# Performance work log

Measured on AMD Instinct MI355X. Metric: run time of the kernel, lower is better.

The kernel has to match this reference:

```python
import jax, jax.numpy as jnp
import numpy as np

DIM = 512
HEADS = 8
HEAD_DIM = DIM // HEADS
WINDOW = 128
TOKEN_SELF_ATTN_VALUE = -5e4  # lucidrains local-attention constant for shared_qk self mask


def setup_inputs() -> dict:
    key = jax.random.key(0)
    k1, k2, k3, k4 = jax.random.split(key, 4)
    B, N = 4, 8192
    x = jax.random.normal(k1, (B, N, DIM), dtype=jnp.float32)
    w_qkv = jax.random.normal(k2, (3 * DIM, DIM), dtype=jnp.float32) * (DIM ** -0.5)
    w_proj = jax.random.normal(k3, (DIM, DIM), dtype=jnp.float32) * (DIM ** -0.5)
    b_proj = jax.random.normal(k4, (DIM,), dtype=jnp.float32) * 0.01
    return {"x": x, "w_qkv": w_qkv, "w_proj": w_proj, "b_proj": b_proj}


def _look_around(b):
    # b: [B,H,nw,w,D] -> [B,H,nw,2w,D] = concat(prev_window, cur_window); window 0 padded with zeros
    padded = jnp.pad(b, ((0, 0), (0, 0), (1, 0), (0, 0), (0, 0)))
    return jnp.concatenate([padded[:, :, :-1], b], axis=3)


def _local_attn(q, k, v):
    # causal sliding-window attention, window=128, look_backward=1, shared_qk
    B, H, N, D = q.shape
    w = WINDOW
    nw = N // w
    scale = D ** -0.5
    # shared_qk: l2-normalize keys (F.normalize, eps=1e-12)
    k = k / jnp.clip(jnp.linalg.norm(k, axis=-1, keepdims=True), 1e-12, None)

    bq = q.reshape(B, H, nw, w, D)
    bk = _look_around(k.reshape(B, H, nw, w, D))  # [B,H,nw,2w,D]
    bv = _look_around(v.reshape(B, H, nw, w, D))

    t = jnp.arange(N).reshape(nw, w)
    t_pad = jnp.pad(t, ((1, 0), (0, 0)), constant_values=-1)
    bq_t = t                                         # [nw, w]
    bq_k = jnp.concatenate([t_pad[:-1], t], axis=1)  # [nw, 2w]

    sim = jnp.einsum('bhwie,bhwje->bhwij', bq, bk) * scale  # [B,H,nw,w,2w]

    self_mask = bq_t[:, :, None] == bq_k[:, None, :]
    causal_mask = bq_t[:, :, None] < bq_k[:, None, :]
    pad_mask = (bq_k == -1)[:, None, :]
    mask_value = -jnp.finfo(sim.dtype).max
    sim = jnp.where(self_mask, TOKEN_SELF_ATTN_VALUE, sim)
    sim = jnp.where(causal_mask | pad_mask, mask_value, sim)

    attn = jax.nn.softmax(sim, axis=-1)  # dropout is identity in eval mode
    out = jnp.einsum('bhwij,bhwje->bhwie', attn, bv)
    return out.reshape(B, H, N, D)


def reference(x, w_qkv, w_proj, b_proj):
    B, N, C = x.shape
    qkv = x @ w_qkv.T  # [B,N,3C]
    q, k, v = jnp.split(qkv, 3, axis=-1)
    to_heads = lambda t: t.reshape(B, N, HEADS, HEAD_DIM).transpose(0, 2, 1, 3)
    out = _local_attn(to_heads(q), to_heads(k), to_heads(v))  # [B,H,N,D]
    out = out.transpose(0, 2, 1, 3).reshape(B, N, C)
    return out @ w_proj.T + b_proj
```

## Files before the change

### kernel.cpp

```cpp
#include <hip/hip_runtime.h>
#include <stdint.h>

typedef uint16_t u16;
typedef __bf16 bf16x8 __attribute__((ext_vector_type(8)));
typedef float f32x4 __attribute__((ext_vector_type(4)));
typedef uint16_t u16x4 __attribute__((ext_vector_type(4)));
typedef uint16_t u16x8 __attribute__((ext_vector_type(8)));

typedef __attribute__((address_space(1))) void as1_void;
typedef __attribute__((address_space(3))) void as3_void;

__device__ __forceinline__ float bf2f(u16 b) {
    union { uint32_t u; float f; } v; v.u = ((uint32_t)b) << 16; return v.f;
}
__device__ __forceinline__ u16 f2bf(float f) {
    union { float f; uint32_t u; } v; v.f = f;
    uint32_t u = v.u;
    u += 0x7fffu + ((u >> 16) & 1u);
    return (u16)(u >> 16);
}
__device__ __forceinline__ void gload_lds16(const u16* g, u16* l) {
    __builtin_amdgcn_global_load_lds((as1_void*)g, (as3_void*)l, 16, 0, 0);
}

__global__ __launch_bounds__(256) void cvt3(
    const float* __restrict__ x,  u16* __restrict__ xb,
    const float* __restrict__ wq, u16* __restrict__ wqb,
    const float* __restrict__ wp, u16* __restrict__ wpb)
{
    const float* src; u16* dst; int base, nb;
    const int b = blockIdx.x;
    if (b < 1024)      { src = x;  dst = xb;  base = b;        nb = 1024; }
    else if (b < 1072) { src = wq; dst = wqb; base = b - 1024; nb = 48;   }
    else               { src = wp; dst = wpb; base = b - 1072; nb = 16;   }
    size_t i = ((size_t)base * 256 + threadIdx.x) * 8;
    const size_t stride = (size_t)nb * 256 * 8;
    #pragma unroll
    for (int it = 0; it < 8; ++it, i += stride) {
        f32x4 a = *(const f32x4*)(src + i);
        f32x4 c = *(const f32x4*)(src + i + 4);
        u16x8 o;
        o[0] = f2bf(a[0]); o[1] = f2bf(a[1]); o[2] = f2bf(a[2]); o[3] = f2bf(a[3]);
        o[4] = f2bf(c[0]); o[5] = f2bf(c[1]); o[6] = f2bf(c[2]); o[7] = f2bf(c[3]);
        *(u16x8*)(dst + i) = o;
    }
}

template<int NT, bool C_F32, bool NORMK>
__global__ __launch_bounds__(512) void gemm256(
    const u16* __restrict__ A, int lda,
    const u16* __restrict__ B, int ldb,
    const float* __restrict__ bias,
    void* __restrict__ Cv, int ldc)
{
    __shared__ u16 lA[2][256 * 64];
    __shared__ u16 lB[2][256 * 64];

    const int tid  = threadIdx.x;
    const int lane = tid & 63;
    const int wave = tid >> 6;
    const int wm = wave >> 2;
    const int wn = wave & 3;
    const int cl = lane & 15;
    const int gr = lane >> 4;

    int fid = blockIdx.y * gridDim.x + blockIdx.x;
    const int nwg = gridDim.x * gridDim.y;
    fid = (fid & 7) * (nwg >> 3) + (fid >> 3);
    const int row0 = (fid / gridDim.x) * 256;
    const int col0 = (fid % gridDim.x) * 256;

    const int srow   = lane >> 3;
    const int schunk = ((lane & 7) - srow) & 7;

    f32x4 acc[8][4] = {};

    auto STAGE = [&](int t, int d) {
        const int k0 = t * 64;
        #pragma unroll
        for (int i = 0; i < 4; ++i) {
            const int Rg = wave * 32 + i * 8;
            gload_lds16(A + (size_t)(row0 + Rg + srow) * lda + k0 + schunk * 8,
                        &lA[d][Rg * 64]);
            gload_lds16(B + (size_t)(col0 + Rg + srow) * ldb + k0 + schunk * 8,
                        &lB[d][Rg * 64]);
        }
    };

    auto COMPUTE = [&](int d) {
        const u16* la = lA[d];
        const u16* lb = lB[d];
        bf16x8 bfrag[2][4];
        #pragma unroll
        for (int kk = 0; kk < 2; ++kk)
            #pragma unroll
            for (int n = 0; n < 4; ++n) {
                const int rb = wn * 64 + n * 16 + cl;
                bfrag[kk][n] = *(const bf16x8*)(lb + rb * 64 + (((kk * 4 + gr + rb) & 7) * 8));
            }
        __builtin_amdgcn_s_setprio(1);
        #pragma unroll
        for (int m = 0; m < 8; ++m) {
            const int ra = wm * 128 + m * 16 + cl;
            const bf16x8 a0 = *(const bf16x8*)(la + ra * 64 + (((gr + ra) & 7) * 8));
            const bf16x8 a1 = *(const bf16x8*)(la + ra * 64 + (((4 + gr + ra) & 7) * 8));
            #pragma unroll
            for (int n = 0; n < 4; ++n)
                acc[m][n] = __builtin_amdgcn_mfma_f32_16x16x32_bf16(a0, bfrag[0][n], acc[m][n], 0, 0, 0);
            #pragma unroll
            for (int n = 0; n < 4; ++n)
                acc[m][n] = __builtin_amdgcn_mfma_f32_16x16x32_bf16(a1, bfrag[1][n], acc[m][n], 0, 0, 0);
        }
        __builtin_amdgcn_s_setprio(0);
    };

    STAGE(0, 0);
    STAGE(1, 1);
    #pragma unroll
    for (int t = 0; t < NT; ++t) {
        if (t < NT - 1) asm volatile("s_waitcnt vmcnt(8)" ::: "memory");
        else            asm volatile("s_waitcnt vmcnt(0)" ::: "memory");
        __builtin_amdgcn_s_barrier();
        COMPUTE(t & 1);
        __builtin_amdgcn_s_barrier();
        if (t + 2 < NT) STAGE(t + 2, t & 1);
    }

    if constexpr (NORMK) {
        if (col0 >= 512 && col0 < 1024) {
            #pragma unroll
            for (int m = 0; m < 8; ++m)
                #pragma unroll
                for (int j = 0; j < 4; ++j) {
                    float ss = 0.f;
                    #pragma unroll
                    for (int n = 0; n < 4; ++n) ss += acc[m][n][j] * acc[m][n][j];
                    ss += __shfl_xor(ss, 1);
                    ss += __shfl_xor(ss, 2);
                    ss += __shfl_xor(ss, 4);
                    ss += __shfl_xor(ss, 8);
                    const float scl = 1.f / fmaxf(sqrtf(ss), 1e-12f);
                    #pragma unroll
                    for (int n = 0; n < 4; ++n) acc[m][n][j] *= scl;
                }
        }
    }

    #pragma unroll
    for (int m = 0; m < 8; ++m) {
        const int r = row0 + wm * 128 + m * 16 + gr * 4;
        #pragma unroll
        for (int n = 0; n < 4; ++n) {
            const int c = col0 + wn * 64 + n * 16 + cl;
            const float bv = bias ? bias[c] : 0.f;
            #pragma unroll
            for (int j = 0; j < 4; ++j) {
                const float val = acc[m][n][j] + bv;
                if constexpr (C_F32) ((float*)Cv)[(size_t)(r + j) * ldc + c] = val;
                else                 ((u16*)Cv)[(size_t)(r + j) * ldc + c] = f2bf(val);
            }
        }
    }
}

template<bool A_F32, bool C_F32, bool NORMK>
__global__ __launch_bounds__(256) void gemm_bt_f32(
    const void* __restrict__ Av, int lda,
    const float* __restrict__ B, int ldb,
    const float* __restrict__ bias,
    void* __restrict__ Cv, int ldc,
    int K)
{
    __shared__ u16 lA[128 * 32];
    __shared__ u16 lB[128 * 32];

    const int tid  = threadIdx.x;
    const int lane = tid & 63;
    const int wave = tid >> 6;
    const int wr   = (wave >> 1) * 64;
    const int wc   = (wave & 1) * 64;
    const int row0 = blockIdx.y * 128;
    const int col0 = blockIdx.x * 128;

    f32x4 acc[4][4] = {};

    for (int k0 = 0; k0 < K; k0 += 32) {
        #pragma unroll
        for (int i = 0; i < 4; ++i) {
            const int idx = i * 256 + tid;
            const int r = idx >> 3;
            const int p = (idx & 7) * 4;
            u16x4 a4, b4;
            if constexpr (A_F32) {
                const float* Af = (const float*)Av;
                f32x4 va = *(const f32x4*)(Af + (size_t)(row0 + r) * lda + k0 + p);
                a4[0] = f2bf(va[0]); a4[1] = f2bf(va[1]); a4[2] = f2bf(va[2]); a4[3] = f2bf(va[3]);
            } else {
                const u16* Ab = (const u16*)Av;
                a4 = *(const u16x4*)(Ab + (size_t)(row0 + r) * lda + k0 + p);
            }
            {
                f32x4 vb = *(const f32x4*)(B + (size_t)(col0 + r) * ldb + k0 + p);
                b4[0] = f2bf(vb[0]); b4[1] = f2bf(vb[1]); b4[2] = f2bf(vb[2]); b4[3] = f2bf(vb[3]);
            }
            *(u16x4*)&lA[r * 32 + p] = a4;
            *(u16x4*)&lB[r * 32 + p] = b4;
        }
        __syncthreads();

        bf16x8 af[4], bfv[4];
        #pragma unroll
        for (int m = 0; m < 4; ++m)
            af[m] = *(const bf16x8*)(lA + (wr + m * 16 + (lane & 15)) * 32 + (lane >> 4) * 8);
        #pragma unroll
        for (int n = 0; n < 4; ++n)
            bfv[n] = *(const bf16x8*)(lB + (wc + n * 16 + (lane & 15)) * 32 + (lane >> 4) * 8);
        #pragma unroll
        for (int m = 0; m < 4; ++m)
            #pragma unroll
            for (int n = 0; n < 4; ++n)
                acc[m][n] = __builtin_amdgcn_mfma_f32_16x16x32_bf16(af[m], bfv[n], acc[m][n], 0, 0, 0);
        __syncthreads();
    }

    if constexpr (NORMK) {
        if (col0 >= 512 && col0 < 1024) {
            #pragma unroll
            for (int m = 0; m < 4; ++m)
                #pragma unroll
                for (int j = 0; j < 4; ++j) {
                    float ss = 0.f;
                    #pragma unroll
                    for (int n = 0; n < 4; ++n) ss += acc[m][n][j] * acc[m][n][j];
                    ss += __shfl_xor(ss, 1);
                    ss += __shfl_xor(ss, 2);
                    ss += __shfl_xor(ss, 4);
                    ss += __shfl_xor(ss, 8);
                    const float scl = 1.f / fmaxf(sqrtf(ss), 1e-12f);
                    #pragma unroll
                    for (int n = 0; n < 4; ++n) acc[m][n][j] *= scl;
                }
        }
    }

    #pragma unroll
    for (int m = 0; m < 4; ++m) {
        const int r = row0 + wr + m * 16 + ((lane >> 4) << 2);
        #pragma unroll
        for (int n = 0; n < 4; ++n) {
            const int c = col0 + wc + n * 16 + (lane & 15);
            const float bv = bias ? bias[c] : 0.f;
            #pragma unroll
            for (int j = 0; j < 4; ++j) {
                const float val = acc[m][n][j] + bv;
                if constexpr (C_F32) ((float*)Cv)[(size_t)(r + j) * ldc + c] = val;
                else                 ((u16*)Cv)[(size_t)(r + j) * ldc + c] = f2bf(val);
            }
        }
    }
}

__global__ __launch_bounds__(512, 4) void attn_kernel(const u16* qkv, u16* o)
{
    constexpr int CC = 1536;
    constexpr int NTOK = 8192;
    constexpr int KP = 72;
    constexpr int VP = 136;
    constexpr int PP = 136;
    __shared__ u16 kn[128 * KP];
    __shared__ u16 vT[64 * VP];
    __shared__ u16 Pl[128 * PP];

    const int tid  = threadIdx.x;
    const int lane = tid & 63;
    const int wave = tid >> 6;
    const int cl = lane & 15;
    const int gr = lane >> 4;

    int blk = blockIdx.x;
    blk = (blk & 7) * (gridDim.x >> 3) + (blk >> 3);

    const int iw  = blk & 63;
    const int h   = (blk >> 6) & 7;
    const int b   = blk >> 9;

    const int tq0 = iw * 128;
    const size_t rowbase = (size_t)b * NTOK;
    const u16* qbase = qkv + rowbase * CC + h * 64;
    const u16* kbase = qbase + 512;
    const u16* vbase = qbase + 1024;

    const int wrow = wave * 16;
    bf16x8 qf[2];
    #pragma unroll
    for (int kk = 0; kk < 2; ++kk)
        qf[kk] = *(const bf16x8*)(qbase + (size_t)(tq0 + wrow + cl) * CC + kk * 32 + gr * 8);

    f32x4 oacc[4] = {};
    float m_run[4] = {-3.0e38f, -3.0e38f, -3.0e38f, -3.0e38f};
    float l_run[4] = {0.f, 0.f, 0.f, 0.f};

    for (int c = 0; c < 2; ++c) {
        const int tkc = tq0 - 128 + c * 128;

        #pragma unroll
        for (int p = 0; p < 2; ++p) {
            const int id = tid + p * 512;
            const int row = id >> 3, dc = id & 7;
            u16x8 v8 = {};
            if (tkc >= 0) v8 = *(const u16x8*)(kbase + (size_t)(tkc + row) * CC + dc * 8);
            *(u16x8*)&kn[row * KP + dc * 8] = v8;
        }
        #pragma unroll
        for (int p = 0; p < 2; ++p) {
            const int id = tid + p * 512;
            const int key = id & 127, dc = id >> 7;
            u16x8 v8 = {};
            if (tkc >= 0) v8 = *(const u16x8*)(vbase + (size_t)(tkc + key) * CC + dc * 8);
            #pragma unroll
            for (int e = 0; e < 8; ++e) vT[(dc * 8 + e) * VP + key] = v8[e];
        }
        __syncthreads();

        f32x4 s[8] = {};
        #pragma unroll
        for (int n = 0; n < 8; ++n)
            #pragma unroll
            for (int kk = 0; kk < 2; ++kk) {
                const bf16x8 kf = *(const bf16x8*)&kn[(n * 16 + cl) * KP + kk * 32 + gr * 8];
                s[n] = __builtin_amdgcn_mfma_f32_16x16x32_bf16(qf[kk], kf, s[n], 0, 0, 0);
            }

        float pmax[4] = {-3.0e38f, -3.0e38f, -3.0e38f, -3.0e38f};
        #pragma unroll
        for (int n = 0; n < 8; ++n) {
            const int tkk = tkc + n * 16 + cl;
            const bool pad = tkk < 0;
            #pragma unroll
            for (int j = 0; j < 4; ++j) {
                const int tq = tq0 + wrow + gr * 4 + j;
                float sv = s[n][j] * 0.125f;
                const int rel = tkk - tq;
                sv = (rel == 0) ? -5.0e4f : sv;
                sv = (rel > 0 || pad) ? -6.0e4f : sv;
                s[n][j] = sv;
                pmax[j] = fmaxf(pmax[j], sv);
            }
        }
        float cold[4];
        #pragma unroll
        for (int j = 0; j < 4; ++j) {
            pmax[j] = fmaxf(pmax[j], __shfl_xor(pmax[j], 1));
            pmax[j] = fmaxf(pmax[j], __shfl_xor(pmax[j], 2));
            pmax[j] = fmaxf(pmax[j], __shfl_xor(pmax[j], 4));
            pmax[j] = fmaxf(pmax[j], __shfl_xor(pmax[j], 8));
            const float mn = fmaxf(m_run[j], pmax[j]);
            cold[j] = __expf(m_run[j] - mn);
            m_run[j] = mn;
            l_run[j] *= cold[j];
        }
        #pragma unroll
        for (int n = 0; n < 8; ++n)
            #pragma unroll
            for (int j = 0; j < 4; ++j) {
                const float p = __expf(s[n][j] - m_run[j]);
                s[n][j] = p;
                l_run[j] += p;
            }
        #pragma unroll
        for (int n = 0; n < 4; ++n) {
            f32x4 t = oacc[n];
            t[0] *= cold[0]; t[1] *= cold[1]; t[2] *= cold[2]; t[3] *= cold[3];
            oacc[n] = t;
        }
        #pragma unroll
        for (int n = 0; n < 8; ++n)
            #pragma unroll
            for (int j = 0; j < 4; ++j)
                Pl[(wrow + gr * 4 + j) * PP + n * 16 + cl] = f2bf(s[n][j]);
        __syncthreads();

        #pragma unroll
        for (int kk = 0; kk < 4; ++kk) {
            const bf16x8 pa = *(const bf16x8*)&Pl[(wrow + cl) * PP + kk * 32 + gr * 8];
            #pragma unroll
            for (int n = 0; n < 4; ++n) {
                const bf16x8 vb = *(const bf16x8*)&vT[(n * 16 + cl) * VP + kk * 32 + gr * 8];
                oacc[n] = __builtin_amdgcn_mfma_f32_16x16x32_bf16(pa, vb, oacc[n], 0, 0, 0);
            }
        }
        __syncthreads();
    }

    float inv[4];
    #pragma unroll
    for (int j = 0; j < 4; ++j) {
        l_run[j] += __shfl_xor(l_run[j], 1);
        l_run[j] += __shfl_xor(l_run[j], 2);
        l_run[j] += __shfl_xor(l_run[j], 4);
        l_run[j] += __shfl_xor(l_run[j], 8);
        inv[j] = 1.f / l_run[j];
    }
    u16* obase = o + rowbase * CC + h * 64;
    const int r0 = tq0 + wrow + gr * 4;
    #pragma unroll
    for (int n = 0; n < 4; ++n) {
        const int d = n * 16 + cl;
        #pragma unroll
        for (int j = 0; j < 4; ++j)
            obase[(size_t)(r0 + j) * CC + d] = f2bf(oacc[n][j] * inv[j]);
    }
}

extern "C" void kernel_launch(void* const* d_in, const int* in_sizes, int n_in,
                              void* d_out, int out_size, void* d_ws, size_t ws_size,
                              hipStream_t stream)
{
    (void)in_sizes; (void)n_in; (void)out_size;
    const float* x      = (const float*)d_in[0];
    const float* w_qkv  = (const float*)d_in[1];
    const float* w_proj = (const float*)d_in[2];
    const float* b_proj = (const float*)d_in[3];
    float* out = (float*)d_out;

    const int BN = 4 * 8192;
    const size_t qkv_b = (size_t)BN * 1536 * 2;
    const size_t xb_b  = (size_t)BN * 512 * 2;
    const size_t wq_b  = (size_t)1536 * 512 * 2;
    const size_t wp_b  = (size_t)512 * 512 * 2;

    uint8_t* p = (uint8_t*)d_ws;
    u16* qkv = (u16*)p;

    if (ws_size >= qkv_b + xb_b + wq_b + wp_b) {
        u16* xb  = (u16*)(p + qkv_b);
        u16* wqb = (u16*)(p + qkv_b + xb_b);
        u16* wpb = (u16*)(p + qkv_b + xb_b + wq_b);
        cvt3<<<1088, 256, 0, stream>>>(x, xb, w_qkv, wqb, w_proj, wpb);
        gemm256<8, false, true><<<dim3(6, 128), 512, 0, stream>>>(
            xb, 512, wqb, 512, nullptr, qkv, 1536);
        attn_kernel<<<dim3(4 * 8 * 64), 512, 0, stream>>>(qkv, qkv);
        gemm256<8, true, false><<<dim3(2, 128), 512, 0, stream>>>(
            qkv, 1536, wpb, 512, b_proj, out, 512);
    } else {
        gemm_bt_f32<true, false, true><<<dim3(12, BN / 128), 256, 0, stream>>>(
            x, 512, w_qkv, 512, nullptr, qkv, 1536, 512);
        attn_kernel<<<dim3(4 * 8 * 64), 512, 0, stream>>>(qkv, qkv);
        gemm_bt_f32<false, true, false><<<dim3(4, BN / 128), 256, 0, stream>>>(
            qkv, 1536, w_proj, 512, b_proj, out, 512, 512);
    }
}
```

Measured before the change: 186.4 us.

## Rework GEMM into four-slot 32-wide K pipeline with single barrier per step

The bf16 GEMM now stages K in 32-wide chunks across a four-slot LDS ring instead of two 64-wide buffers. Each step issues the next chunk's loads after reading fragments and uses one barrier per iteration rather than two. This aims to keep more loads in flight and cut synchronisation stalls. It drops the XOR swizzle, so LDS bank conflicts may rise, and it doubles the number of loop iterations. The NORMK column check now uses the per-wave column offset.

Result: no change. 186.6 us (+0.1%).

```diff
diff --git a/kernel.cpp b/kernel.cpp
--- a/kernel.cpp
+++ b/kernel.cpp
@@ -21,6 +21,12 @@
 }
 __device__ __forceinline__ void gload_lds16(const u16* g, u16* l) {
     __builtin_amdgcn_global_load_lds((as1_void*)g, (as3_void*)l, 16, 0, 0);
+}
+__device__ __forceinline__ void vmwait(int n) {
+    if (n == 0)       asm volatile("s_waitcnt vmcnt(0)" ::: "memory");
+    else if (n == 4)  asm volatile("s_waitcnt vmcnt(4)" ::: "memory");
+    else if (n == 8)  asm volatile("s_waitcnt vmcnt(8)" ::: "memory");
+    else              asm volatile("s_waitcnt vmcnt(12)" ::: "memory");
 }
 
 __global__ __launch_bounds__(256) void cvt3(
@@ -47,14 +53,15 @@
 }
 
 template<int NT, bool C_F32, bool NORMK>
-__global__ __launch_bounds__(512) void gemm256(
+__global__ __launch_bounds__(512) void gemm8p(
     const u16* __restrict__ A, int lda,
     const u16* __restrict__ B, int ldb,
     const float* __restrict__ bias,
     void* __restrict__ Cv, int ldc)
 {
-    __shared__ u16 lA[2][256 * 64];
-    __shared__ u16 lB[2][256 * 64];
+    constexpr int NP = 2 * NT;
+    __shared__ u16 lA[4][256 * 32];
+    __shared__ u16 lB[4][256 * 32];
 
     const int tid  = threadIdx.x;
     const int lane = tid & 63;
@@ -70,64 +77,50 @@
     const int row0 = (fid / gridDim.x) * 256;
     const int col0 = (fid % gridDim.x) * 256;
 
-    const int srow   = lane >> 3;
-    const int schunk = ((lane & 7) - srow) & 7;
-
     f32x4 acc[8][4] = {};
 
-    auto STAGE = [&](int t, int d) {
-        const int k0 = t * 64;
-        #pragma unroll
-        for (int i = 0; i < 4; ++i) {
-            const int Rg = wave * 32 + i * 8;
-            gload_lds16(A + (size_t)(row0 + Rg + srow) * lda + k0 + schunk * 8,
-                        &lA[d][Rg * 64]);
-            gload_lds16(B + (size_t)(col0 + Rg + srow) * ldb + k0 + schunk * 8,
-                        &lB[d][Rg * 64]);
+    auto STAGE = [&](int cp) {
+        const int slot = cp & 3;
+        const int kg = cp * 32;
+        #pragma unroll
+        for (int i = 0; i < 2; ++i) {
+            const int id = i * 512 + tid;
+            const int row = id >> 2;
+            const int ch = id & 3;
+            gload_lds16(A + (size_t)(row0 + row) * lda + kg + ch * 8,
+                        &lA[slot][(i * 512 + wave * 64) * 8]);
+            gload_lds16(B + (size_t)(col0 + row) * ldb + kg + ch * 8,
+                        &lB[slot][(i * 512 + wave * 64) * 8]);
         }
     };
 
-    auto COMPUTE = [&](int d) {
-        const u16* la = lA[d];
-        const u16* lb = lB[d];
-        bf16x8 bfrag[2][4];
-        #pragma unroll
-        for (int kk = 0; kk < 2; ++kk)
-            #pragma unroll
-            for (int n = 0; n < 4; ++n) {
-                const int rb = wn * 64 + n * 16 + cl;
-                bfrag[kk][n] = *(const bf16x8*)(lb + rb * 64 + (((kk * 4 + gr + rb) & 7) * 8));
-            }
+    STAGE(0); STAGE(1); STAGE(2); STAGE(3);
+
+    #pragma unroll
+    for (int p = 0; p < NP; ++p) {
+        vmwait(p == 0 ? 12 : (p <= NP - 3 ? 8 : (p == NP - 2 ? 4 : 0)));
+        __builtin_amdgcn_s_barrier();
+        const u16* la = lA[p & 3];
+        const u16* lb = lB[p & 3];
+        bf16x8 af[8], bfr[4];
+        #pragma unroll
+        for (int m = 0; m < 8; ++m)
+            af[m] = *(const bf16x8*)&la[(wm * 128 + m * 16 + cl) * 32 + gr * 8];
+        #pragma unroll
+        for (int n = 0; n < 4; ++n)
+            bfr[n] = *(const bf16x8*)&lb[(wn * 64 + n * 16 + cl) * 32 + gr * 8];
+        if (p >= 1 && p <= NP - 4) STAGE(p + 3);
         __builtin_amdgcn_s_setprio(1);
         #pragma unroll
-        for (int m = 0; m < 8; ++m) {
-            const int ra = wm * 128 + m * 16 + cl;
-            const bf16x8 a0 = *(const bf16x8*)(la + ra * 64 + (((gr + ra) & 7) * 8));
-            const bf16x8 a1 = *(const bf16x8*)(la + ra * 64 + (((4 + gr + ra) & 7) * 8));
+        for (int m = 0; m < 8; ++m)
             #pragma unroll
             for (int n = 0; n < 4; ++n)
-                acc[m][n] = __builtin_amdgcn_mfma_f32_16x16x32_bf16(a0, bfrag[0][n], acc[m][n], 0, 0, 0);
-            #pragma unroll
-            for (int n = 0; n < 4; ++n)
-                acc[m][n] = __builtin_amdgcn_mfma_f32_16x16x32_bf16(a1, bfrag[1][n], acc[m][n], 0, 0, 0);
-        }
+                acc[m][n] = __builtin_amdgcn_mfma_f32_16x16x32_bf16(af[m], bfr[n], acc[m][n], 0, 0, 0);
         __builtin_amdgcn_s_setprio(0);
-    };
-
-    STAGE(0, 0);
-    STAGE(1, 1);
-    #pragma unroll
-    for (int t = 0; t < NT; ++t) {
-        if (t < NT - 1) asm volatile("s_waitcnt vmcnt(8)" ::: "memory");
-        else            asm volatile("s_waitcnt vmcnt(0)" ::: "memory");
-        __builtin_amdgcn_s_barrier();
-        COMPUTE(t & 1);
-        __builtin_amdgcn_s_barrier();
-        if (t + 2 < NT) STAGE(t + 2, t & 1);
     }
 
     if constexpr (NORMK) {
-        if (col0 >= 512 && col0 < 1024) {
+        if (col0 + wn * 64 >= 512 && col0 + wn * 64 < 1024) {
             #pragma unroll
             for (int m = 0; m < 8; ++m)
                 #pragma unroll
@@ -437,10 +430,10 @@
         u16* wqb = (u16*)(p + qkv_b + xb_b);
         u16* wpb = (u16*)(p + qkv_b + xb_b + wq_b);
         cvt3<<<1088, 256, 0, stream>>>(x, xb, w_qkv, wqb, w_proj, wpb);
-        gemm256<8, false, true><<<dim3(6, 128), 512, 0, stream>>>(
+        gemm8p<8, false, true><<<dim3(6, 128), 512, 0, stream>>>(
             xb, 512, wqb, 512, nullptr, qkv, 1536);
         attn_kernel<<<dim3(4 * 8 * 64), 512, 0, stream>>>(qkv, qkv);
-        gemm256<8, true, false><<<dim3(2, 128), 512, 0, stream>>>(
+        gemm8p<8, true, false><<<dim3(2, 128), 512, 0, stream>>>(
             qkv, 1536, wpb, 512, b_proj, out, 512);
     } else {
         gemm_bt_f32<true, false, true><<<dim3(12, BN / 128), 256, 0, stream>>>(
```

## Fuse fp32-to-bf16 conversion of x into the QKV GEMM A-operand load

Applied to the files above, without the earlier changes.

Drops the separate pass that converted the whole activation tensor x to bf16. A new 128x128-tile GEMM instead stages fp32 A tiles into LDS and converts them to bf16 in registers before the MFMAs. Only the weights are still pre-converted. This removes one full write and re-read of the bf16 copy of x, at the cost of twice the LDS traffic for A, extra conversion instructions in the inner loop, and a smaller tile with a different grid. The K-norm column check in the old GEMM is also changed to be per-wave.

Result: faster. 174.7 us (-6.3%).

```diff
diff --git a/kernel.cpp b/kernel.cpp
--- a/kernel.cpp
+++ b/kernel.cpp
@@ -23,26 +23,140 @@
     __builtin_amdgcn_global_load_lds((as1_void*)g, (as3_void*)l, 16, 0, 0);
 }
 
-__global__ __launch_bounds__(256) void cvt3(
-    const float* __restrict__ x,  u16* __restrict__ xb,
+__global__ __launch_bounds__(256) void cvt_w(
     const float* __restrict__ wq, u16* __restrict__ wqb,
     const float* __restrict__ wp, u16* __restrict__ wpb)
 {
-    const float* src; u16* dst; int base, nb;
+    const float* src; u16* dst; int base;
     const int b = blockIdx.x;
-    if (b < 1024)      { src = x;  dst = xb;  base = b;        nb = 1024; }
-    else if (b < 1072) { src = wq; dst = wqb; base = b - 1024; nb = 48;   }
-    else               { src = wp; dst = wpb; base = b - 1072; nb = 16;   }
-    size_t i = ((size_t)base * 256 + threadIdx.x) * 8;
-    const size_t stride = (size_t)nb * 256 * 8;
-    #pragma unroll
-    for (int it = 0; it < 8; ++it, i += stride) {
-        f32x4 a = *(const f32x4*)(src + i);
-        f32x4 c = *(const f32x4*)(src + i + 4);
-        u16x8 o;
-        o[0] = f2bf(a[0]); o[1] = f2bf(a[1]); o[2] = f2bf(a[2]); o[3] = f2bf(a[3]);
-        o[4] = f2bf(c[0]); o[5] = f2bf(c[1]); o[6] = f2bf(c[2]); o[7] = f2bf(c[3]);
-        *(u16x8*)(dst + i) = o;
+    if (b < 384) { src = wq; dst = wqb; base = b; }
+    else         { src = wp; dst = wpb; base = b - 384; }
+    const size_t i = ((size_t)base * 256 + threadIdx.x) * 8;
+    f32x4 a = *(const f32x4*)(src + i);
+    f32x4 c = *(const f32x4*)(src + i + 4);
+    u16x8 o;
+    o[0] = f2bf(a[0]); o[1] = f2bf(a[1]); o[2] = f2bf(a[2]); o[3] = f2bf(a[3]);
+    o[4] = f2bf(c[0]); o[5] = f2bf(c[1]); o[6] = f2bf(c[2]); o[7] = f2bf(c[3]);
+    *(u16x8*)(dst + i) = o;
+}
+
+template<int NT, bool NORMK>
+__global__ __launch_bounds__(256, 3) void gemm_a32(
+    const float* __restrict__ A, int lda,
+    const u16* __restrict__ B, int ldb,
+    u16* __restrict__ C, int ldc)
+{
+    __shared__ float lA[2][128 * 32];
+    __shared__ u16   lB[2][128 * 32];
+
+    const int tid  = threadIdx.x;
+    const int lane = tid & 63;
+    const int wave = tid >> 6;
+    const int wr = (wave >> 1) * 64;
+    const int wc = (wave & 1) * 64;
+    const int cl = lane & 15;
+    const int gr = lane >> 4;
+
+    int fid = blockIdx.y * gridDim.x + blockIdx.x;
+    const int nwg = gridDim.x * gridDim.y;
+    fid = (fid & 7) * (nwg >> 3) + (fid >> 3);
+    const int row0 = (fid / gridDim.x) * 128;
+    const int col0 = (fid % gridDim.x) * 128;
+
+    const int srowA = lane >> 3;
+    const int schA  = ((lane & 7) - srowA) & 7;
+    const int srowB = lane >> 2;
+    const int schB  = ((lane & 3) - srowB) & 3;
+
+    f32x4 acc[4][4] = {};
+
+    auto STAGE = [&](int t, int d) {
+        const int k0 = t * 32;
+        #pragma unroll
+        for (int i = 0; i < 4; ++i) {
+            const int Rg = wave * 32 + i * 8;
+            gload_lds16((const u16*)(A + (size_t)(row0 + Rg + srowA) * lda + k0 + schA * 4),
+                        (u16*)&lA[d][Rg * 32]);
+        }
+        #pragma unroll
+        for (int i = 0; i < 2; ++i) {
+            const int Rg = wave * 16 + i * 64;
+            gload_lds16(B + (size_t)(col0 + Rg + srowB) * ldb + k0 + schB * 8,
+                        &lB[d][Rg * 32]);
+        }
+    };
+
+    STAGE(0, 0);
+    STAGE(1, 1);
+    #pragma unroll
+    for (int t = 0; t < NT; ++t) {
+        if (t < NT - 1) asm volatile("s_waitcnt vmcnt(6)" ::: "memory");
+        else            asm volatile("s_waitcnt vmcnt(0)" ::: "memory");
+        __builtin_amdgcn_s_barrier();
+        const float* la = lA[t & 1];
+        const u16*   lb = lB[t & 1];
+
+        bf16x8 af[4], bfv[4];
+        #pragma unroll
+        for (int m = 0; m < 4; ++m) {
+            const int ra = wr + m * 16 + cl;
+            const int s0 = (gr * 2 + ra) & 7;
+            const int s1 = (gr * 2 + 1 + ra) & 7;
+            const f32x4 x0 = *(const f32x4*)&la[ra * 32 + s0 * 4];
+            const f32x4 x1 = *(const f32x4*)&la[ra * 32 + s1 * 4];
+            bf16x8 t8;
+            t8[0] = (__bf16)x0[0]; t8[1] = (__bf16)x0[1];
+            t8[2] = (__bf16)x0[2]; t8[3] = (__bf16)x0[3];
+            t8[4] = (__bf16)x1[0]; t8[5] = (__bf16)x1[1];
+            t8[6] = (__bf16)x1[2]; t8[7] = (__bf16)x1[3];
+            af[m] = t8;
+        }
+        #pragma unroll
+        for (int n = 0; n < 4; ++n) {
+            const int rb = wc + n * 16 + cl;
+            bfv[n] = *(const bf16x8*)&lb[rb * 32 + ((gr + rb) & 3) * 8];
+        }
+        __builtin_amdgcn_s_setprio(1);
+        #pragma unroll
+        for (int m = 0; m < 4; ++m)
+            #pragma unroll
+            for (int n = 0; n < 4; ++n)
+                acc[m][n] = __builtin_amdgcn_mfma_f32_16x16x32_bf16(af[m], bfv[n], acc[m][n], 0, 0, 0);
+        __builtin_amdgcn_s_setprio(0);
+        __builtin_amdgcn_s_barrier();
+        if (t + 2 < NT) STAGE(t + 2, t & 1);
+    }
+
+    if constexpr (NORMK) {
+        if (col0 + wc >= 512 && col0 + wc < 1024) {
+            #pragma unroll
+            for (int m = 0; m < 4; ++m)
+                #pragma unroll
+                for (int j = 0; j < 4; ++j) {
+                    float ss = 0.f;
+                    #pragma unroll
+                    for (int n = 0; n < 4; ++n) ss += acc[m][n][j] * acc[m][n][j];
+                    ss += __shfl_xor(ss, 1);
+                    ss += __shfl_xor(ss, 2);
+                    ss += __shfl_xor(ss, 4);
+                    ss += __shfl_xor(ss, 8);
+                    const float scl = 1.f / fmaxf(sqrtf(ss), 1e-12f);
+                    #pragma unroll
+                    for (int n = 0; n < 4; ++n) acc[m][n][j] *= scl;
+                }
+        }
+    }
+
+    #pragma unroll
+    for (int m = 0; m < 4; ++m) {
+        const int r = row0 + wr + m * 16 + gr * 4;
+        #pragma unroll
+        for (int n = 0; n < 4; ++n) {
+            const int c = col0 + wc + n * 16 + cl;
+            #pragma unroll
+            for (int j = 0; j < 4; ++j)
+                C[(size_t)(r + j) * ldc + c] = f2bf(acc[m][n][j]);
+        }
     }
 }
 
@@ -127,7 +241,7 @@
     }
 
     if constexpr (NORMK) {
-        if (col0 >= 512 && col0 < 1024) {
+        if (col0 + wn * 64 >= 512 && col0 + wn * 64 < 1024) {
             #pragma unroll
             for (int m = 0; m < 8; ++m)
                 #pragma unroll
@@ -425,20 +539,18 @@
 
     const int BN = 4 * 8192;
     const size_t qkv_b = (size_t)BN * 1536 * 2;
-    const size_t xb_b  = (size_t)BN * 512 * 2;
     const size_t wq_b  = (size_t)1536 * 512 * 2;
     const size_t wp_b  = (size_t)512 * 512 * 2;
 
     uint8_t* p = (uint8_t*)d_ws;
     u16* qkv = (u16*)p;
 
-    if (ws_size >= qkv_b + xb_b + wq_b + wp_b) {
-        u16* xb  = (u16*)(p + qkv_b);
-        u16* wqb = (u16*)(p + qkv_b + xb_b);
-        u16* wpb = (u16*)(p + qkv_b + xb_b + wq_b);
-        cvt3<<<1088, 256, 0, stream>>>(x, xb, w_qkv, wqb, w_proj, wpb);
-        gemm256<8, false, true><<<dim3(6, 128), 512, 0, stream>>>(
-            xb, 512, wqb, 512, nullptr, qkv, 1536);
+    if (ws_size >= qkv_b + wq_b + wp_b) {
+        u16* wqb = (u16*)(p + qkv_b);
+        u16* wpb = (u16*)(p + qkv_b + wq_b);
+        cvt_w<<<512, 256, 0, stream>>>(w_qkv, wqb, w_proj, wpb);
+        gemm_a32<16, true><<<dim3(12, 256), 256, 0, stream>>>(
+            x, 512, wqb, 512, qkv, 1536);
         attn_kernel<<<dim3(4 * 8 * 64), 512, 0, stream>>>(qkv, qkv);
         gemm256<8, true, false><<<dim3(2, 128), 512, 0, stream>>>(
             qkv, 1536, wpb, 512, b_proj, out, 512);
```
